# Kernel optimization log

Hardware: AMD Instinct MI355X
Metric: run time of the kernel (lower is better)

## Reference

```python
import jax, jax.numpy as jnp
import numpy as np

EPS = 1e-5
DIM = 128
SCALE = DIM ** (-0.5)


def setup_inputs() -> dict:
    key = jax.random.key(0)
    k1, k2, k3 = jax.random.split(key, 3)
    B, N, D = 2, 128 * 128, DIM
    Q = N // 4
    x = jax.random.normal(k1, (B, N, D), dtype=jnp.float32)
    gamma = jnp.ones((D,), dtype=jnp.float32)
    beta = jnp.zeros((D,), dtype=jnp.float32)
    queries = jax.random.normal(k2, (Q, D), dtype=jnp.float32)
    W = jax.random.normal(k3, (2 * D, D), dtype=jnp.float32) * (1.0 / np.sqrt(D))
    return {"x": x, "gamma": gamma, "beta": beta, "queries": queries, "W": W}


def reference(x, gamma, beta, queries, W):
    # LayerNorm over last dim (eps matches torch default 1e-5)
    mu = jnp.mean(x, axis=-1, keepdims=True)
    var = jnp.mean(jnp.square(x - mu), axis=-1, keepdims=True)
    xn = (x - mu) * jax.lax.rsqrt(var + EPS) * gamma + beta  # [B, N, D]
    # learned-query cross attention: sim = Q @ xn^T * scale -> softmax -> @ xn
    sim = jnp.einsum('qd,bnd->bqn', queries, xn) * SCALE     # [B, Q, N]
    attn = jax.nn.softmax(sim, axis=-1)
    out = jnp.einsum('bqn,bnd->bqd', attn, xn)               # [B, Q, D]
    # trailing linear: dim -> 2*dim, no bias
    return jnp.einsum('bqd,ed->bqe', out, W)                 # [B, Q, 2D]
```

## Files before the change

### kernel.cpp

```cpp
#include <hip/hip_runtime.h>
#include <stdint.h>

#define Nn 16384
#define Dd 128
#define Qq 4096
#define Ee 256
#define NSPLIT 8
#define NCHUNK 2048
#define KV 64
#define NITER 32

typedef __bf16 bf16x8 __attribute__((ext_vector_type(8)));
typedef float floatx16 __attribute__((ext_vector_type(16)));
typedef unsigned uintx2 __attribute__((ext_vector_type(2)));

__device__ __forceinline__ float fexp2(float x) {
#if __has_builtin(__builtin_amdgcn_exp2f)
  return __builtin_amdgcn_exp2f(x);
#else
  return exp2f(x);
#endif
}
__device__ __forceinline__ unsigned pk_bf(float lo, float hi) {
  return __builtin_amdgcn_perm(__float_as_uint(hi) + 0x8000u,
                               __float_as_uint(lo) + 0x8000u, 0x07060302u);
}
__device__ __forceinline__ void stage16(const void* g, void* lds_uniform) {
  __builtin_amdgcn_global_load_lds(
      (const __attribute__((address_space(1))) unsigned int*)g,
      (__attribute__((address_space(3))) unsigned int*)lds_uniform, 16, 0, 0);
}
__device__ __forceinline__ void plswap(unsigned a, unsigned b, int hi,
                                       unsigned& r0, unsigned& r1) {
#if __has_builtin(__builtin_amdgcn_permlane32_swap)
  uintx2 r = __builtin_amdgcn_permlane32_swap(a, b, false, false);
  r0 = r[0];
  r1 = r[1];
  (void)hi;
#else
  unsigned ax = __shfl_xor(a, 32);
  unsigned bx = __shfl_xor(b, 32);
  r0 = hi ? bx : a;
  r1 = hi ? b : ax;
#endif
}

__global__ __launch_bounds__(256) void k_lnt(
    const float* __restrict__ x, const float* __restrict__ gamma,
    const float* __restrict__ beta, const float* __restrict__ queries,
    const float* __restrict__ W, unsigned* __restrict__ xn,
    unsigned short* __restrict__ xnT, unsigned short* __restrict__ qb,
    unsigned short* __restrict__ wb) {
  __shared__ __align__(16) uint2 lds2[64 * 32];
  const int tid = threadIdx.x;
  const int bid = blockIdx.x;
  const int b = bid >> 8, n0 = (bid & 255) * 64;
  const int r = tid >> 2, qd = tid & 3;

  const float4* xp = (const float4*)(x + ((size_t)(b * Nn + n0 + r)) * Dd + qd * 32);
  float4 v[8];
  float s = 0.f, s2 = 0.f;
#pragma unroll
  for (int i = 0; i < 8; ++i) {
    v[i] = xp[i];
    s += (v[i].x + v[i].y) + (v[i].z + v[i].w);
    s2 += (v[i].x * v[i].x + v[i].y * v[i].y) + (v[i].z * v[i].z + v[i].w * v[i].w);
  }
  s += __shfl_xor(s, 1); s2 += __shfl_xor(s2, 1);
  s += __shfl_xor(s, 2); s2 += __shfl_xor(s2, 2);
  float mu = s * (1.0f / 128.0f);
  float var = s2 * (1.0f / 128.0f) - mu * mu;
  float rs = rsqrtf(var + 1e-5f);

  const float4* gp = (const float4*)(gamma + qd * 32);
  const float4* bp = (const float4*)(beta + qd * 32);
  unsigned pk[16];
#pragma unroll
  for (int i = 0; i < 8; ++i) {
    float4 g = gp[i], bt = bp[i];
    pk[2 * i] = pk_bf((v[i].x - mu) * rs * g.x + bt.x, (v[i].y - mu) * rs * g.y + bt.y);
    pk[2 * i + 1] = pk_bf((v[i].z - mu) * rs * g.z + bt.z, (v[i].w - mu) * rs * g.w + bt.w);
  }
  unsigned* xrow = xn + ((size_t)(b * Nn + n0 + r)) * 64;
#pragma unroll
  for (int j = 0; j < 4; ++j)
    *(uint4*)(xrow + (((qd * 4 + j) ^ (r & 7)) * 4)) =
        make_uint4(pk[4 * j], pk[4 * j + 1], pk[4 * j + 2], pk[4 * j + 3]);
  const int rk = r & 31;
#pragma unroll
  for (int kk = 0; kk < 8; ++kk)
    lds2[r * 32 + ((qd * 8 + kk) ^ rk)] = make_uint2(pk[2 * kk], pk[2 * kk + 1]);
  __syncthreads();
  const int dq = tid >> 3, nc = tid & 7;
  uint2 U[8];
#pragma unroll
  for (int j = 0; j < 8; ++j) {
    int rr = nc * 8 + j;
    U[j] = lds2[rr * 32 + (dq ^ (rr & 31))];
  }
#pragma unroll
  for (int e = 0; e < 4; ++e) {
    int d = dq * 4 + e;
    unsigned a0 = (e & 2) ? U[0].y : U[0].x, a1 = (e & 2) ? U[1].y : U[1].x;
    unsigned a2 = (e & 2) ? U[2].y : U[2].x, a3 = (e & 2) ? U[3].y : U[3].x;
    unsigned a4 = (e & 2) ? U[4].y : U[4].x, a5 = (e & 2) ? U[5].y : U[5].x;
    unsigned a6 = (e & 2) ? U[6].y : U[6].x, a7 = (e & 2) ? U[7].y : U[7].x;
    unsigned sel = (e & 1) ? 0x07060302u : 0x05040100u;
    uint4 o;
    o.x = __builtin_amdgcn_perm(a1, a0, sel);
    o.y = __builtin_amdgcn_perm(a3, a2, sel);
    o.z = __builtin_amdgcn_perm(a5, a4, sel);
    o.w = __builtin_amdgcn_perm(a7, a6, sel);
    *(uint4*)(xnT + ((size_t)(b * Dd + d)) * Nn + n0 + (nc ^ (d & 7)) * 8) = o;
  }
  const float QSC = 0.08838834764831845f * 1.4426950408889634f;
  const int total4 = (Qq * Dd + Ee * Dd) / 4;
  for (int u = bid * 256 + tid; u < total4; u += 512 * 256) {
    if (u < Qq * Dd / 4) {
      float4 v4 = ((const float4*)queries)[u];
      ((uint2*)qb)[u] = make_uint2(pk_bf(v4.x * QSC, v4.y * QSC),
                                   pk_bf(v4.z * QSC, v4.w * QSC));
    } else {
      float4 v4 = ((const float4*)W)[u - Qq * Dd / 4];
      ((uint2*)wb)[u - Qq * Dd / 4] =
          make_uint2(pk_bf(v4.x, v4.y), pk_bf(v4.z, v4.w));
    }
  }
}

__global__ __launch_bounds__(256, 2) void k_attn(
    const unsigned short* __restrict__ xn,
    const unsigned short* __restrict__ xnT,
    const unsigned short* __restrict__ qb,
    float* __restrict__ o_part,
    float* __restrict__ l_part) {
  __shared__ __align__(16) char lds[2][32768];

  const int bid = blockIdx.x;
  const int split = bid & 7, qt = (bid >> 3) & 31, b = bid >> 8;
  const int tid = threadIdx.x;
  const int wave = tid >> 6, lane = tid & 63;
  const int col = lane & 31, half = lane >> 5;
  const int ck = col & 7;
  const int qwbase = qt * 128 + wave * 32;

  bf16x8 qf[8];
#pragma unroll
  for (int s = 0; s < 8; ++s)
    qf[s] = *(const bf16x8*)(qb + (size_t)(qwbase + col) * Dd + s * 16 + half * 8);

  const floatx16 fz = {0.f,0.f,0.f,0.f,0.f,0.f,0.f,0.f,0.f,0.f,0.f,0.f,0.f,0.f,0.f,0.f};
  floatx16 O[4];
#pragma unroll
  for (int d = 0; d < 4; ++d) O[d] = fz;
  float lsum = 0.f;

  const char* gx = (const char*)xn + (size_t)b * Nn * 256;
  const char* gxt = (const char*)xnT + (size_t)b * Dd * Nn * 2;

  {
    const int nb = split * NCHUNK;
    const char* xsrc = gx + (size_t)nb * 256;
#pragma unroll
    for (int p = 0; p < 4; ++p) {
      int m = wave * 4 + p;
      stage16(xsrc + m * 1024 + lane * 16, &lds[0][0] + m * 1024);
    }
#pragma unroll
    for (int p = 0; p < 4; ++p) {
      int m = wave * 4 + p;
      const char* g = gxt + (size_t)(m * 8 + (lane >> 3)) * (Nn * 2) +
                      (size_t)nb * 2 + (lane & 7) * 16;
      stage16(g, &lds[0][0] + 16384 + m * 1024);
    }
  }
  asm volatile("s_waitcnt vmcnt(0)" ::: "memory");
  __builtin_amdgcn_s_barrier();

  int cur = 0;
#pragma unroll 1
  for (int i = 0; i < NITER; ++i) {
    if (i + 1 < NITER) {
      char* bufn = &lds[0][0] + ((cur ^ 1) << 15);
      const int nb = split * NCHUNK + (i + 1) * KV;
      const char* xsrc = gx + (size_t)nb * 256;
#pragma unroll
      for (int p = 0; p < 4; ++p) {
        int m = wave * 4 + p;
        stage16(xsrc + m * 1024 + lane * 16, bufn + m * 1024);
      }
#pragma unroll
      for (int p = 0; p < 4; ++p) {
        int m = wave * 4 + p;
        const char* g = gxt + (size_t)(m * 8 + (lane >> 3)) * (Nn * 2) +
                        (size_t)nb * 2 + (lane & 7) * 16;
        stage16(g, bufn + 16384 + m * 1024);
      }
    }
    const char* lx = &lds[0][0] + (cur << 15);
    const char* lxt = lx + 16384;

    floatx16 S[2];
    S[0] = fz; S[1] = fz;
    __builtin_amdgcn_s_setprio(1);
#pragma unroll
    for (int s = 0; s < 8; ++s)
#pragma unroll
      for (int mt = 0; mt < 2; ++mt) {
        bf16x8 ax = *(const bf16x8*)(lx + (32 * mt + col) * 256 +
                                     (((2 * s + half) ^ ck) * 16));
        S[mt] = __builtin_amdgcn_mfma_f32_32x32x16_bf16(ax, qf[s], S[mt], 0, 0, 0);
      }
    __builtin_amdgcn_s_setprio(0);

    unsigned P[2][4][2];
#pragma unroll
    for (int mt = 0; mt < 2; ++mt)
#pragma unroll
      for (int t = 0; t < 4; ++t) {
        float p0 = fexp2(S[mt][4 * t]);
        float p1 = fexp2(S[mt][4 * t + 1]);
        float p2 = fexp2(S[mt][4 * t + 2]);
        float p3 = fexp2(S[mt][4 * t + 3]);
        lsum += (p0 + p1) + (p2 + p3);
        P[mt][t][0] = pk_bf(p0, p1);
        P[mt][t][1] = pk_bf(p2, p3);
      }

    __builtin_amdgcn_s_setprio(1);
#pragma unroll
    for (int s2 = 0; s2 < 4; ++s2) {
      const int mt = s2 >> 1, ge = 2 * (s2 & 1), go = ge + 1;
      unsigned w0, w1, w2, w3;
      plswap(P[mt][ge][0], P[mt][go][0], half, w0, w2);
      plswap(P[mt][ge][1], P[mt][go][1], half, w1, w3);
      union { uint4 u; bf16x8 v; } ap;
      ap.u = make_uint4(w0, w1, w2, w3);
#pragma unroll
      for (int dn = 0; dn < 4; ++dn) {
        bf16x8 bx = *(const bf16x8*)(lxt + (32 * dn + col) * 128 +
                                     (((2 * s2 + half) ^ ck) * 16));
        O[dn] = __builtin_amdgcn_mfma_f32_32x32x16_bf16(ap.v, bx, O[dn], 0, 0, 0);
      }
    }
    __builtin_amdgcn_s_setprio(0);

    if (i + 1 < NITER) {
      asm volatile("s_waitcnt vmcnt(0)" ::: "memory");
      __builtin_amdgcn_s_barrier();
    }
    cur ^= 1;
  }

  float lt = lsum + __shfl_xor(lsum, 32);
  if (half == 0)
    l_part[(size_t)(b * NSPLIT + split) * Qq + qwbase + col] = lt;
  float* op = o_part + ((size_t)(b * NSPLIT + split) * Qq + qwbase) * Dd;
#pragma unroll
  for (int dn = 0; dn < 4; ++dn)
#pragma unroll
    for (int r = 0; r < 16; ++r) {
      int q = (r & 3) + 8 * (r >> 2) + 4 * half;
      op[(size_t)q * Dd + dn * 32 + col] = O[dn][r];
    }
}

__global__ __launch_bounds__(256) void k_comb(
    const float* __restrict__ o_part, const float* __restrict__ l_part,
    const unsigned short* __restrict__ wb, float* __restrict__ out) {
  __shared__ __align__(16) char lds_a[32 * 256];
  __shared__ float lds_linv[32];
  const int bid = blockIdx.x;
  const int b = bid >> 7, qc = bid & 127;
  const int qbase = qc * 32;
  const int tid = threadIdx.x;
  const int wave = tid >> 6, lane = tid & 63;
  const int col = lane & 31, half = lane >> 5;
  const int ck = col & 7;

  if (tid < 32) {
    float l = 0.f;
#pragma unroll
    for (int s = 0; s < 8; ++s)
      l += l_part[(size_t)(b * 8 + s) * Qq + qbase + tid];
    lds_linv[tid] = 1.0f / l;
  }
  __syncthreads();

#pragma unroll
  for (int i = 0; i < 4; ++i) {
    int idx = i * 256 + tid;
    int q = idx >> 5, d4 = idx & 31;
    float4 acc = make_float4(0.f, 0.f, 0.f, 0.f);
#pragma unroll
    for (int s = 0; s < 8; ++s) {
      float4 v = *(const float4*)(o_part + ((size_t)(b * 8 + s) * Qq + qbase + q) * Dd + d4 * 4);
      acc.x += v.x; acc.y += v.y; acc.z += v.z; acc.w += v.w;
    }
    float li = lds_linv[q];
    int w = d4 >> 1;
    int pos = (w & 8) | ((w ^ (q & 7)) & 7);
    *(uint2*)(lds_a + q * 256 + pos * 16 + (d4 & 1) * 8) =
        make_uint2(pk_bf(acc.x * li, acc.y * li), pk_bf(acc.z * li, acc.w * li));
  }
  __syncthreads();

  bf16x8 af[8];
#pragma unroll
  for (int s = 0; s < 8; ++s) {
    int u = 2 * s + half;
    int pos = (u & 8) | ((u ^ ck) & 7);
    af[s] = *(const bf16x8*)(lds_a + col * 256 + pos * 16);
  }

  const floatx16 fz = {0.f,0.f,0.f,0.f,0.f,0.f,0.f,0.f,0.f,0.f,0.f,0.f,0.f,0.f,0.f,0.f};
#pragma unroll
  for (int et = 0; et < 2; ++et) {
    floatx16 C = fz;
    int e_row = wave * 64 + et * 32 + col;
#pragma unroll
    for (int s = 0; s < 8; ++s) {
      bf16x8 bw = *(const bf16x8*)(wb + (size_t)e_row * Dd + s * 16 + half * 8);
      C = __builtin_amdgcn_mfma_f32_32x32x16_bf16(af[s], bw, C, 0, 0, 0);
    }
#pragma unroll
    for (int r = 0; r < 16; ++r) {
      int q = qbase + (r & 3) + 8 * (r >> 2) + 4 * half;
      out[((size_t)b * Qq + q) * Ee + wave * 64 + et * 32 + col] = C[r];
    }
  }
}

extern "C" void kernel_launch(void* const* d_in, const int* in_sizes, int n_in,
                              void* d_out, int out_size, void* d_ws, size_t ws_size,
                              hipStream_t stream) {
  const float* x = (const float*)d_in[0];
  const float* gamma = (const float*)d_in[1];
  const float* beta = (const float*)d_in[2];
  const float* queries = (const float*)d_in[3];
  const float* W = (const float*)d_in[4];
  float* out = (float*)d_out;

  char* w = (char*)d_ws;
  unsigned short* xn = (unsigned short*)(w);
  unsigned short* xnT = (unsigned short*)(w + 8388608);
  unsigned short* qb = (unsigned short*)(w + 16777216);
  unsigned short* wb = (unsigned short*)(w + 17825792);
  float* o_part = (float*)(w + 17891328);
  float* l_part = (float*)(w + 51445760);

  k_lnt<<<dim3(512), dim3(256), 0, stream>>>(x, gamma, beta, queries, W,
                                             (unsigned*)xn, xnT, qb, wb);
  k_attn<<<dim3(512), dim3(256), 0, stream>>>(xn, xnT, qb, o_part, l_part);
  k_comb<<<dim3(256), dim3(256), 0, stream>>>(o_part, l_part, wb, out);
}
```

Before: 160.5 us.

## Template attention kernel on split count and waves; use 16 splits with 8-wave blocks

Parameterizes the attention kernel by the number of N-splits and waves per block. When the workspace is large enough it uses 16 splits with 512-thread blocks, each covering 256 queries, and keeps the old 8-split, 4-wave path as a fallback. Each staged K/V tile is now shared by twice as many query rows, which halves global and LDS traffic per query, and the shorter per-split loop lets blocks finish sooner. The cost is twice as much partial-output data for the combine kernel to write and read, plus higher register and occupancy pressure from the larger blocks.

Measured after the change: 222.4 us. +38.6%, slower.

```diff
diff --git a/kernel.cpp b/kernel.cpp
--- a/kernel.cpp
+++ b/kernel.cpp
@@ -5,10 +5,7 @@
 #define Dd 128
 #define Qq 4096
 #define Ee 256
-#define NSPLIT 8
-#define NCHUNK 2048
 #define KV 64
-#define NITER 32
 
 typedef __bf16 bf16x8 __attribute__((ext_vector_type(8)));
 typedef float floatx16 __attribute__((ext_vector_type(16)));
@@ -128,21 +125,28 @@
   }
 }
 
-__global__ __launch_bounds__(256, 2) void k_attn(
+template <int NS, int NWAVE>
+__global__ __launch_bounds__(NWAVE * 64, NWAVE / 2) void k_attn(
     const unsigned short* __restrict__ xn,
     const unsigned short* __restrict__ xnT,
     const unsigned short* __restrict__ qb,
     float* __restrict__ o_part,
     float* __restrict__ l_part) {
+  constexpr int NCH = Nn / NS;
+  constexpr int NIT = NCH / KV;
+  constexpr int QT = Qq / (32 * NWAVE);
+  constexpr int CPW = 16 / NWAVE;
   __shared__ __align__(16) char lds[2][32768];
 
   const int bid = blockIdx.x;
-  const int split = bid & 7, qt = (bid >> 3) & 31, b = bid >> 8;
+  const int split = bid % NS;
+  const int qt = (bid / NS) % QT;
+  const int b = bid / (NS * QT);
   const int tid = threadIdx.x;
   const int wave = tid >> 6, lane = tid & 63;
   const int col = lane & 31, half = lane >> 5;
   const int ck = col & 7;
-  const int qwbase = qt * 128 + wave * 32;
+  const int qwbase = qt * (32 * NWAVE) + wave * 32;
 
   bf16x8 qf[8];
 #pragma unroll
@@ -159,16 +163,16 @@
   const char* gxt = (const char*)xnT + (size_t)b * Dd * Nn * 2;
 
   {
-    const int nb = split * NCHUNK;
+    const int nb = split * NCH;
     const char* xsrc = gx + (size_t)nb * 256;
 #pragma unroll
-    for (int p = 0; p < 4; ++p) {
-      int m = wave * 4 + p;
+    for (int p = 0; p < CPW; ++p) {
+      int m = wave * CPW + p;
       stage16(xsrc + m * 1024 + lane * 16, &lds[0][0] + m * 1024);
     }
 #pragma unroll
-    for (int p = 0; p < 4; ++p) {
-      int m = wave * 4 + p;
+    for (int p = 0; p < CPW; ++p) {
+      int m = wave * CPW + p;
       const char* g = gxt + (size_t)(m * 8 + (lane >> 3)) * (Nn * 2) +
                       (size_t)nb * 2 + (lane & 7) * 16;
       stage16(g, &lds[0][0] + 16384 + m * 1024);
@@ -179,19 +183,19 @@
 
   int cur = 0;
 #pragma unroll 1
-  for (int i = 0; i < NITER; ++i) {
-    if (i + 1 < NITER) {
+  for (int i = 0; i < NIT; ++i) {
+    if (i + 1 < NIT) {
       char* bufn = &lds[0][0] + ((cur ^ 1) << 15);
-      const int nb = split * NCHUNK + (i + 1) * KV;
+      const int nb = split * NCH + (i + 1) * KV;
       const char* xsrc = gx + (size_t)nb * 256;
 #pragma unroll
-      for (int p = 0; p < 4; ++p) {
-        int m = wave * 4 + p;
+      for (int p = 0; p < CPW; ++p) {
+        int m = wave * CPW + p;
         stage16(xsrc + m * 1024 + lane * 16, bufn + m * 1024);
       }
 #pragma unroll
-      for (int p = 0; p < 4; ++p) {
-        int m = wave * 4 + p;
+      for (int p = 0; p < CPW; ++p) {
+        int m = wave * CPW + p;
         const char* g = gxt + (size_t)(m * 8 + (lane >> 3)) * (Nn * 2) +
                         (size_t)nb * 2 + (lane & 7) * 16;
         stage16(g, bufn + 16384 + m * 1024);
@@ -245,7 +249,7 @@
     }
     __builtin_amdgcn_s_setprio(0);
 
-    if (i + 1 < NITER) {
+    if (i + 1 < NIT) {
       asm volatile("s_waitcnt vmcnt(0)" ::: "memory");
       __builtin_amdgcn_s_barrier();
     }
@@ -254,8 +258,8 @@
 
   float lt = lsum + __shfl_xor(lsum, 32);
   if (half == 0)
-    l_part[(size_t)(b * NSPLIT + split) * Qq + qwbase + col] = lt;
-  float* op = o_part + ((size_t)(b * NSPLIT + split) * Qq + qwbase) * Dd;
+    l_part[(size_t)(b * NS + split) * Qq + qwbase + col] = lt;
+  float* op = o_part + ((size_t)(b * NS + split) * Qq + qwbase) * Dd;
 #pragma unroll
   for (int dn = 0; dn < 4; ++dn)
 #pragma unroll
@@ -265,6 +269,7 @@
     }
 }
 
+template <int NS>
 __global__ __launch_bounds__(256) void k_comb(
     const float* __restrict__ o_part, const float* __restrict__ l_part,
     const unsigned short* __restrict__ wb, float* __restrict__ out) {
@@ -281,8 +286,8 @@
   if (tid < 32) {
     float l = 0.f;
 #pragma unroll
-    for (int s = 0; s < 8; ++s)
-      l += l_part[(size_t)(b * 8 + s) * Qq + qbase + tid];
+    for (int s = 0; s < NS; ++s)
+      l += l_part[(size_t)(b * NS + s) * Qq + qbase + tid];
     lds_linv[tid] = 1.0f / l;
   }
   __syncthreads();
@@ -293,8 +298,8 @@
     int q = idx >> 5, d4 = idx & 31;
     float4 acc = make_float4(0.f, 0.f, 0.f, 0.f);
 #pragma unroll
-    for (int s = 0; s < 8; ++s) {
-      float4 v = *(const float4*)(o_part + ((size_t)(b * 8 + s) * Qq + qbase + q) * Dd + d4 * 4);
+    for (int s = 0; s < NS; ++s) {
+      float4 v = *(const float4*)(o_part + ((size_t)(b * NS + s) * Qq + qbase + q) * Dd + d4 * 4);
       acc.x += v.x; acc.y += v.y; acc.z += v.z; acc.w += v.w;
     }
     float li = lds_linv[q];
@@ -346,11 +351,19 @@
   unsigned short* xnT = (unsigned short*)(w + 8388608);
   unsigned short* qb = (unsigned short*)(w + 16777216);
   unsigned short* wb = (unsigned short*)(w + 17825792);
-  float* o_part = (float*)(w + 17891328);
-  float* l_part = (float*)(w + 51445760);
 
   k_lnt<<<dim3(512), dim3(256), 0, stream>>>(x, gamma, beta, queries, W,
                                              (unsigned*)xn, xnT, qb, wb);
-  k_attn<<<dim3(512), dim3(256), 0, stream>>>(xn, xnT, qb, o_part, l_part);
-  k_comb<<<dim3(256), dim3(256), 0, stream>>>(o_part, l_part, wb, out);
-}
+
+  if (ws_size >= 85524480ull) {
+    float* o_part = (float*)(w + 17891328);
+    float* l_part = (float*)(w + 17891328 + 67108864);
+    k_attn<16, 8><<<dim3(512), dim3(512), 0, stream>>>(xn, xnT, qb, o_part, l_part);
+    k_comb<16><<<dim3(256), dim3(256), 0, stream>>>(o_part, l_part, wb, out);
+  } else {
+    float* o_part = (float*)(w + 17891328);
+    float* l_part = (float*)(w + 51445760);
+    k_attn<8, 4><<<dim3(512), dim3(256), 0, stream>>>(xn, xnT, qb, o_part, l_part);
+    k_comb<8><<<dim3(256), dim3(256), 0, stream>>>(o_part, l_part, wb, out);
+  }
+}
```
